# Kernel optimization log

Measured on AMD Instinct MI355X. Metric: run time of the kernel, lower is better.

The kernel has to match this reference:

```python
import jax, jax.numpy as jnp
import numpy as np

B, S, D = 32, 256, 768
H = 12
HD = D // H           # 64
MLP = 4 * D           # 3072
EPS = 1e-5


def layernorm(x, g, b):
    mu = jnp.mean(x, axis=-1, keepdims=True)
    var = jnp.mean((x - mu) ** 2, axis=-1, keepdims=True)
    return (x - mu) * jax.lax.rsqrt(var + EPS) * g + b


def setup_inputs() -> dict:
    key = jax.random.key(0)
    ks = jax.random.split(key, 16)
    s_head = 1.0 / np.sqrt(HD)
    s_d = 1.0 / np.sqrt(D)
    s_mlp = 1.0 / np.sqrt(MLP)
    return {
        "x": jax.random.normal(ks[0], (B, S, D), dtype=jnp.float32),
        "g1": jnp.ones((D,), jnp.float32),
        "beta1": jnp.zeros((D,), jnp.float32),
        # per-head linear weights, torch Linear layout [out, in] stacked over heads
        "Wq": jax.random.uniform(ks[1], (H, HD, HD), jnp.float32, -s_head, s_head),
        "bq": jax.random.uniform(ks[2], (H, HD), jnp.float32, -s_head, s_head),
        "Wk": jax.random.uniform(ks[3], (H, HD, HD), jnp.float32, -s_head, s_head),
        "bk": jax.random.uniform(ks[4], (H, HD), jnp.float32, -s_head, s_head),
        "Wv": jax.random.uniform(ks[5], (H, HD, HD), jnp.float32, -s_head, s_head),
        "bv": jax.random.uniform(ks[6], (H, HD), jnp.float32, -s_head, s_head),
        "g2": jnp.ones((D,), jnp.float32),
        "beta2": jnp.zeros((D,), jnp.float32),
        "W1": jax.random.uniform(ks[7], (MLP, D), jnp.float32, -s_d, s_d),
        "bm1": jax.random.uniform(ks[8], (MLP,), jnp.float32, -s_d, s_d),
        "W2": jax.random.uniform(ks[9], (D, MLP), jnp.float32, -s_mlp, s_mlp),
        "bm2": jax.random.uniform(ks[10], (D,), jnp.float32, -s_mlp, s_mlp),
    }


def reference(x, g1, beta1, Wq, bq, Wk, bk, Wv, bv, g2, beta2, W1, bm1, W2, bm2):
    # --- MHA on norm1(x), fused over batch and heads ---
    h = layernorm(x, g1, beta1)                      # [B,S,D]
    hh = h.reshape(B, S, H, HD)                      # head split matches slicing in Mymha
    # q_e = sum_d hh_d * W[e,d]  (torch Linear: y = x @ W.T + b)
    q = jnp.einsum('bshd,hed->bshe', hh, Wq) + bq
    k = jnp.einsum('bshd,hed->bshe', hh, Wk) + bk
    v = jnp.einsum('bshd,hed->bshe', hh, Wv) + bv
    scores = jnp.einsum('bshe,bthe->bhst', q, k) / np.sqrt(HD)
    attn = jax.nn.softmax(scores, axis=-1)           # [B,H,S,S]
    ctx = jnp.einsum('bhst,bthe->bshe', attn, v).reshape(B, S, D)
    out = ctx + x
    # --- MLP on norm2(out) ---
    h2 = layernorm(out, g2, beta2)
    m = jax.nn.gelu(h2 @ W1.T + bm1, approximate=False)  # torch nn.GELU is exact erf
    out = m @ W2.T + bm2 + out
    return out
```

## Files before the change

### kernel.cpp

```cpp
#include <hip/hip_runtime.h>
#include <hip/hip_bf16.h>
#include <math.h>


static constexpr int Bn = 32, Sn = 256, Dn = 768, Hn = 12, HDn = 64, MLPn = 3072;
static constexpr int NT = Bn * Sn;

typedef unsigned short ushort_t;
typedef unsigned int u32;
typedef __attribute__((ext_vector_type(8))) short short8;
typedef __attribute__((ext_vector_type(4))) float f32x4;

__device__ __forceinline__ float bf2f(ushort_t u) { return __uint_as_float(((u32)u) << 16); }
__device__ __forceinline__ ushort_t f2bf(float f) {
  u32 u = __float_as_uint(f);
  u += 0x7fffu + ((u >> 16) & 1u);
  return (ushort_t)(u >> 16);
}

__device__ __forceinline__ void async_cp16(const ushort_t* g, ushort_t* l) {
  __builtin_amdgcn_global_load_lds(
      (const __attribute__((address_space(1))) u32*)g,
      (__attribute__((address_space(3))) u32*)l, 16, 0, 0);
}

__global__ __launch_bounds__(256) void k_prep(
    const float* __restrict__ Wq, const float* __restrict__ Wk,
    const float* __restrict__ Wv, const float* __restrict__ bq,
    const float* __restrict__ bk, const float* __restrict__ bv,
    const float* __restrict__ W1, const float* __restrict__ W2,
    const float* __restrict__ x, const float* __restrict__ g1,
    const float* __restrict__ be1,
    ushort_t* __restrict__ Wc, float* __restrict__ bc,
    ushort_t* __restrict__ W1b, ushort_t* __restrict__ W2b,
    ushort_t* __restrict__ hb)
{
  __shared__ float red[8];
  const int bx = blockIdx.x;
  const int tid = threadIdx.x;
  if (bx < 576) {
    int i = bx * 256 + tid;
    int h = i / 12288, rem = i - h * 12288;
    int mat = rem / 4096, w = rem - mat * 4096;
    const float* src = (mat == 0) ? Wq : ((mat == 1) ? Wk : Wv);
    Wc[i] = f2bf(src[h * 4096 + w]);
    if (i < Hn * 192) {
      int h2 = i / 192, r2 = i - h2 * 192;
      int m2 = r2 / 64, e2 = r2 - m2 * 64;
      const float* bs = (m2 == 0) ? bq : ((m2 == 1) ? bk : bv);
      bc[i] = bs[h2 * 64 + e2];
    }
  } else if (bx < 5184) {
    int j = bx - 576;
    const float* src = (j < 2304) ? W1 : W2;
    ushort_t* dst = (j < 2304) ? W1b : W2b;
    int i = (j % 2304) * 256 + tid;
    float4 v = ((const float4*)src)[i];
    ushort4 o;
    o.x = f2bf(v.x); o.y = f2bf(v.y); o.z = f2bf(v.z); o.w = f2bf(v.w);
    ((ushort4*)dst)[i] = o;
  } else {
    const int t = bx - 5184;
    float xv[3];
#pragma unroll
    for (int i = 0; i < 3; i++) xv[i] = x[(size_t)t * Dn + tid + i * 256];
    float s = xv[0] + xv[1] + xv[2];
#pragma unroll
    for (int off = 32; off > 0; off >>= 1) s += __shfl_down(s, off, 64);
    if ((tid & 63) == 0) red[tid >> 6] = s;
    __syncthreads();
    float mean = (red[0] + red[1] + red[2] + red[3]) * (1.0f / 768.0f);
    float d0 = xv[0] - mean, d1 = xv[1] - mean, d2 = xv[2] - mean;
    float s2 = d0 * d0 + d1 * d1 + d2 * d2;
#pragma unroll
    for (int off = 32; off > 0; off >>= 1) s2 += __shfl_down(s2, off, 64);
    if ((tid & 63) == 0) red[4 + (tid >> 6)] = s2;
    __syncthreads();
    float rstd = rsqrtf((red[4] + red[5] + red[6] + red[7]) * (1.0f / 768.0f) + 1e-5f);
#pragma unroll
    for (int i = 0; i < 3; i++) {
      int d = tid + i * 256;
      hb[(size_t)t * Dn + d] = f2bf((xv[i] - mean) * rstd * g1[d] + be1[d]);
    }
  }
}

__global__ __launch_bounds__(256) void k_fused(
    const ushort_t* __restrict__ hb,
    const ushort_t* __restrict__ Wc,
    const float* __restrict__ bc,
    const float* __restrict__ x,
    float* __restrict__ out1)
{
  __shared__ __align__(16) ushort_t smem[77824];
  ushort_t* Qs  = smem;
  ushort_t* Ks  = smem + 16384;
  ushort_t* Vts = smem + 32768;
  ushort_t* As  = smem + 49152;
  ushort_t* Ws  = smem + 65536;
  ushort_t* Pw  = smem + 49152;

  const int bh = blockIdx.x;
  const int b_ = bh / Hn, h_ = bh - b_ * Hn;
  const int tid = threadIdx.x;
  const int wave = tid >> 6, lane = tid & 63;
  const int lrow = lane & 15, quad = lane >> 4;
  const int key = lrow & 7;
  const int t0 = b_ * Sn;

  {
    const ushort_t* ga = hb + (size_t)t0 * Dn + h_ * 64;
#pragma unroll
    for (int j = 0; j < 8; ++j) {
      int q = j * 256 + tid;
      int row = q >> 3;
      int sc = (q & 7) ^ (row & 7);
      async_cp16(ga + (size_t)row * Dn + sc * 8, As + q * 8);
    }
    const ushort_t* gw = Wc + h_ * 12288;
#pragma unroll
    for (int j = 0; j < 6; ++j) {
      int q = j * 256 + tid;
      int row = q >> 3;
      int sc = (q & 7) ^ (row & 7);
      async_cp16(gw + row * 64 + sc * 8, Ws + q * 8);
    }
  }
  asm volatile("s_waitcnt vmcnt(0)" ::: "memory");
  __syncthreads();

  const int wm = (wave >> 1) * 64, wn = (wave & 1) * 96;
  for (int half = 0; half < 2; ++half) {
    f32x4 acc[4][6];
#pragma unroll
    for (int mi = 0; mi < 4; mi++)
#pragma unroll
      for (int ni = 0; ni < 6; ni++) acc[mi][ni] = (f32x4){0.f, 0.f, 0.f, 0.f};

#pragma unroll
    for (int kk = 0; kk < 2; kk++) {
      short8 af[4], wf[6];
#pragma unroll
      for (int mi = 0; mi < 4; mi++)
        af[mi] = *(const short8*)(As + (half * 128 + wm + mi * 16 + lrow) * 64 + ((((kk << 2) + quad)) ^ key) * 8);
#pragma unroll
      for (int ni = 0; ni < 6; ni++)
        wf[ni] = *(const short8*)(Ws + (wn + ni * 16 + lrow) * 64 + ((((kk << 2) + quad)) ^ key) * 8);
#pragma unroll
      for (int mi = 0; mi < 4; mi++)
#pragma unroll
        for (int ni = 0; ni < 6; ni++)
          acc[mi][ni] = __builtin_amdgcn_mfma_f32_16x16x32_bf16(af[mi], wf[ni], acc[mi][ni], 0, 0, 0);
    }

#pragma unroll
    for (int ni = 0; ni < 6; ni++) {
      int c = wn + ni * 16 + lrow;
      int mat = c >> 6, e = c & 63;
      float bb = bc[h_ * 192 + c];
      if (mat < 2) {
        ushort_t* dst = (mat == 0) ? Qs : Ks;
#pragma unroll
        for (int mi = 0; mi < 4; mi++) {
#pragma unroll
          for (int r = 0; r < 4; r++) {
            int srow = half * 128 + wm + mi * 16 + quad * 4 + r;
            dst[srow * 64 + (((e >> 3) ^ (srow & 7)) << 3) + (e & 7)] = f2bf(acc[mi][ni][r] + bb);
          }
        }
      } else {
#pragma unroll
        for (int mi = 0; mi < 4; mi++) {
          int c4 = half * 128 + wm + mi * 16 + quad * 4;
          ushort4 pk;
          pk.x = f2bf(acc[mi][ni][0] + bb);
          pk.y = f2bf(acc[mi][ni][1] + bb);
          pk.z = f2bf(acc[mi][ni][2] + bb);
          pk.w = f2bf(acc[mi][ni][3] + bb);
          int cq = c4 >> 3;
          *(ushort4*)(Vts + e * 256 + ((cq ^ (e & 7)) << 3) + (c4 & 7)) = pk;
        }
      }
    }
  }
  __syncthreads();

  ushort_t* Pme = Pw + wave * 4224;
  for (int p = 0; p < 4; ++p) {
    const int s0 = wave * 64 + p * 16;
    short8 qf[2];
#pragma unroll
    for (int kk = 0; kk < 2; kk++)
      qf[kk] = *(const short8*)(Qs + (s0 + lrow) * 64 + ((((kk << 2) + quad)) ^ key) * 8);

    f32x4 sc[16];
#pragma unroll
    for (int ni = 0; ni < 16; ni++) sc[ni] = (f32x4){0.f, 0.f, 0.f, 0.f};
#pragma unroll
    for (int kk = 0; kk < 2; kk++) {
#pragma unroll
      for (int ni = 0; ni < 16; ni++) {
        short8 kf = *(const short8*)(Ks + (ni * 16 + lrow) * 64 + ((((kk << 2) + quad)) ^ key) * 8);
        sc[ni] = __builtin_amdgcn_mfma_f32_16x16x32_bf16(qf[kk], kf, sc[ni], 0, 0, 0);
      }
    }

    float inv[4];
#pragma unroll
    for (int r = 0; r < 4; r++) {
      float m_ = sc[0][r];
#pragma unroll
      for (int ni = 1; ni < 16; ni++) m_ = fmaxf(m_, sc[ni][r]);
#pragma unroll
      for (int msk = 8; msk >= 1; msk >>= 1) m_ = fmaxf(m_, __shfl_xor(m_, msk, 64));
      float s_ = 0.f;
#pragma unroll
      for (int ni = 0; ni < 16; ni++) {
        float pv = __expf((sc[ni][r] - m_) * 0.125f);
        s_ += pv;
        Pme[(quad * 4 + r) * 264 + ni * 16 + lrow] = f2bf(pv);
      }
#pragma unroll
      for (int msk = 8; msk >= 1; msk >>= 1) s_ += __shfl_xor(s_, msk, 64);
      inv[r] = 1.0f / s_;
    }
    asm volatile("s_waitcnt lgkmcnt(0)" ::: "memory");
    __builtin_amdgcn_sched_barrier(0);

    f32x4 of[4];
#pragma unroll
    for (int et = 0; et < 4; et++) of[et] = (f32x4){0.f, 0.f, 0.f, 0.f};
#pragma unroll
    for (int ks = 0; ks < 8; ks++) {
      short8 pf = *(const short8*)(Pme + lrow * 264 + ks * 32 + quad * 8);
#pragma unroll
      for (int et = 0; et < 4; et++) {
        short8 vf = *(const short8*)(Vts + (et * 16 + lrow) * 256 + ((((ks << 2) + quad)) ^ key) * 8);
        of[et] = __builtin_amdgcn_mfma_f32_16x16x32_bf16(pf, vf, of[et], 0, 0, 0);
      }
    }

    const size_t obase = ((size_t)t0 + s0) * Dn + h_ * 64;
#pragma unroll
    for (int r = 0; r < 4; r++) {
      float rl = inv[r];
      int row = quad * 4 + r;
#pragma unroll
      for (int et = 0; et < 4; et++) {
        size_t idx = obase + (size_t)row * Dn + et * 16 + lrow;
        out1[idx] = of[et][r] * rl + x[idx];
      }
    }
  }
}

__global__ __launch_bounds__(256) void k_ln2(
    const float* __restrict__ in, const float* __restrict__ g2,
    const float* __restrict__ be2, ushort_t* __restrict__ h2)
{
  const int t = blockIdx.x, tid = threadIdx.x;
  __shared__ float red[8];
  float xv[3];
#pragma unroll
  for (int i = 0; i < 3; i++) xv[i] = in[(size_t)t * Dn + tid + i * 256];
  float s = xv[0] + xv[1] + xv[2];
#pragma unroll
  for (int off = 32; off > 0; off >>= 1) s += __shfl_down(s, off, 64);
  if ((tid & 63) == 0) red[tid >> 6] = s;
  __syncthreads();
  float mean = (red[0] + red[1] + red[2] + red[3]) * (1.0f / 768.0f);
  float d0 = xv[0] - mean, d1 = xv[1] - mean, d2 = xv[2] - mean;
  float s2 = d0 * d0 + d1 * d1 + d2 * d2;
#pragma unroll
  for (int off = 32; off > 0; off >>= 1) s2 += __shfl_down(s2, off, 64);
  if ((tid & 63) == 0) red[4 + (tid >> 6)] = s2;
  __syncthreads();
  float rstd = rsqrtf((red[4] + red[5] + red[6] + red[7]) * (1.0f / 768.0f) + 1e-5f);
#pragma unroll
  for (int i = 0; i < 3; i++) {
    int d = tid + i * 256;
    h2[(size_t)t * Dn + d] = f2bf((xv[i] - mean) * rstd * g2[d] + be2[d]);
  }
}

__global__ __launch_bounds__(512, 2) void k_gemm1(
    const ushort_t* __restrict__ A,
    const ushort_t* __restrict__ Bw,
    const float* __restrict__ bias,
    ushort_t* __restrict__ CoutB)
{
  constexpr int KD = Dn;
  constexpr int NTILES = 12;
  constexpr int BUFU = 28672;
  __shared__ __align__(16) ushort_t smem[57344];
  const int b = blockIdx.x;
  const int xcd = b & 7, slot = b >> 3;
  const int cc = slot % 16, rloc = slot / 16;
  const int m0 = (xcd * 4 + rloc) * 256, n0 = cc * 192;
  const int tid = threadIdx.x;
  const int wave = tid >> 6, lane = tid & 63;
  const int wm2 = (wave >> 2) * 128, wn2 = (wave & 3) * 48;
  const int lrow = lane & 15, quad = lane >> 4;
  const int key = lrow & 7;

  f32x4 acc[8][3];
#pragma unroll
  for (int mi = 0; mi < 8; mi++)
#pragma unroll
    for (int ni = 0; ni < 3; ni++) acc[mi][ni] = (f32x4){0.f, 0.f, 0.f, 0.f};

  auto stageA = [&](int t, int half) {
    if (t >= NTILES) return;
    const int k0 = t * 64;
    ushort_t* tb = smem + (t & 1) * BUFU + half * 8192;
#pragma unroll
    for (int j = 0; j < 2; ++j) {
      int q = j * 512 + tid;
      int row = q >> 3;
      int sc = (q & 7) ^ (row & 7);
      async_cp16(A + (size_t)(m0 + half * 128 + row) * KD + k0 + sc * 8, tb + q * 8);
    }
  };
  auto stageB = [&](int t) {
    if (t >= NTILES) return;
    const int k0 = t * 64;
    ushort_t* tb = smem + (t & 1) * BUFU + 16384;
#pragma unroll
    for (int j = 0; j < 3; ++j) {
      int q = j * 512 + tid;
      int row = q >> 3;
      int sc = (q & 7) ^ (row & 7);
      async_cp16(Bw + (size_t)(n0 + row) * KD + k0 + sc * 8, tb + q * 8);
    }
  };

  stageA(0, 0); stageA(0, 1); stageB(0);
  asm volatile("s_waitcnt vmcnt(0)" ::: "memory");
  __builtin_amdgcn_s_barrier();
  __builtin_amdgcn_sched_barrier(0);

  short8 af[4][2], af2[4][2], bf0[3], bf1[3];
  for (int t = 0; t < NTILES; ++t) {
    const ushort_t* Ab = smem + (t & 1) * BUFU;
    const ushort_t* Bb = Ab + 16384;

#pragma unroll
    for (int mi = 0; mi < 4; ++mi)
#pragma unroll
      for (int kk = 0; kk < 2; ++kk)
        af[mi][kk] = *(const short8*)(Ab + (wm2 + mi * 16 + lrow) * 64 + (((kk << 2) + quad) ^ key) * 8);
#pragma unroll
    for (int ni = 0; ni < 3; ++ni)
      bf0[ni] = *(const short8*)(Bb + (wn2 + ni * 16 + lrow) * 64 + ((quad ^ key) * 8));
    stageA(t + 1, 0);
    __builtin_amdgcn_s_barrier();
    asm volatile("s_waitcnt lgkmcnt(0)" ::: "memory");
    __builtin_amdgcn_sched_barrier(0);
    __builtin_amdgcn_s_setprio(1);
#pragma unroll
    for (int mi = 0; mi < 4; ++mi)
#pragma unroll
      for (int ni = 0; ni < 3; ++ni)
        acc[mi][ni] = __builtin_amdgcn_mfma_f32_16x16x32_bf16(af[mi][0], bf0[ni], acc[mi][ni], 0, 0, 0);
    __builtin_amdgcn_s_setprio(0);
    __builtin_amdgcn_s_barrier();
    __builtin_amdgcn_sched_barrier(0);

#pragma unroll
    for (int ni = 0; ni < 3; ++ni)
      bf1[ni] = *(const short8*)(Bb + (wn2 + ni * 16 + lrow) * 64 + (((4 + quad) ^ key) * 8));
#pragma unroll
    for (int mi = 0; mi < 4; ++mi)
#pragma unroll
      for (int kk = 0; kk < 2; ++kk)
        af2[mi][kk] = *(const short8*)(Ab + (wm2 + 64 + mi * 16 + lrow) * 64 + (((kk << 2) + quad) ^ key) * 8);
    stageA(t + 1, 1);
    __builtin_amdgcn_s_barrier();
    asm volatile("s_waitcnt lgkmcnt(0)" ::: "memory");
    __builtin_amdgcn_sched_barrier(0);
    __builtin_amdgcn_s_setprio(1);
#pragma unroll
    for (int mi = 0; mi < 4; ++mi)
#pragma unroll
      for (int ni = 0; ni < 3; ++ni)
        acc[mi][ni] = __builtin_amdgcn_mfma_f32_16x16x32_bf16(af[mi][1], bf1[ni], acc[mi][ni], 0, 0, 0);
    __builtin_amdgcn_s_setprio(0);
    __builtin_amdgcn_s_barrier();
    __builtin_amdgcn_sched_barrier(0);

    stageB(t + 1);
    __builtin_amdgcn_s_barrier();
    __builtin_amdgcn_sched_barrier(0);
    __builtin_amdgcn_s_setprio(1);
#pragma unroll
    for (int mi = 0; mi < 4; ++mi)
#pragma unroll
      for (int ni = 0; ni < 3; ++ni)
        acc[4 + mi][ni] = __builtin_amdgcn_mfma_f32_16x16x32_bf16(af2[mi][0], bf0[ni], acc[4 + mi][ni], 0, 0, 0);
    __builtin_amdgcn_s_setprio(0);
    __builtin_amdgcn_s_barrier();
    __builtin_amdgcn_sched_barrier(0);

    __builtin_amdgcn_s_setprio(1);
#pragma unroll
    for (int mi = 0; mi < 4; ++mi)
#pragma unroll
      for (int ni = 0; ni < 3; ++ni)
        acc[4 + mi][ni] = __builtin_amdgcn_mfma_f32_16x16x32_bf16(af2[mi][1], bf1[ni], acc[4 + mi][ni], 0, 0, 0);
    __builtin_amdgcn_s_setprio(0);
    asm volatile("s_waitcnt vmcnt(0)" ::: "memory");
    __builtin_amdgcn_s_barrier();
    __builtin_amdgcn_sched_barrier(0);
  }

  float bwv[3];
#pragma unroll
  for (int ni = 0; ni < 3; ++ni) bwv[ni] = bias[n0 + wn2 + ni * 16 + lrow];
  __syncthreads();
#pragma unroll
  for (int mi = 0; mi < 8; ++mi) {
#pragma unroll
    for (int ni = 0; ni < 3; ++ni) {
      int col = wn2 + ni * 16 + lrow;
#pragma unroll
      for (int r = 0; r < 4; ++r) {
        int row = wm2 + mi * 16 + quad * 4 + r;
        float vv = acc[mi][ni][r] + bwv[ni];
        float u = vv * (0.7978845608f + 0.0356774081f * vv * vv);
        float o = vv / (1.0f + __expf(-2.0f * u));
        smem[row * 200 + col] = f2bf(o);
      }
    }
  }
  __syncthreads();
#pragma unroll
  for (int i = 0; i < 12; ++i) {
    int idx = i * 512 + tid;
    int rr = idx / 24, ck = idx - rr * 24;
    const uint4 v = *(const uint4*)(smem + rr * 200 + ck * 8);
    *(uint4*)(CoutB + (size_t)(m0 + rr) * MLPn + n0 + ck * 8) = v;
  }
}

__global__ __launch_bounds__(512, 2) void k_gemm2(
    const ushort_t* __restrict__ A,
    const ushort_t* __restrict__ Bw,
    const float* __restrict__ bias,
    const float* __restrict__ res,
    float* __restrict__ out)
{
  constexpr int KD = MLPn;
  constexpr int N = Dn;
  constexpr int NTILES = 48;
  constexpr int BUFU = 20480;
  __shared__ __align__(16) ushort_t smem[61440];
  const int b = blockIdx.x;
  const int xcd = b & 7, slot = b >> 3;
  const int cc = slot & 3, rloc = slot >> 2;
  const int m0 = (xcd * 8 + rloc) * 128, n0 = cc * 192;
  const int tid = threadIdx.x;
  const int wave = tid >> 6, lane = tid & 63;
  const int wm2 = (wave >> 2) * 64, wn2 = (wave & 3) * 48;
  const int lrow = lane & 15, quad = lane >> 4;
  const int key = lrow & 7;

  f32x4 acc[4][3];
#pragma unroll
  for (int mi = 0; mi < 4; mi++)
#pragma unroll
    for (int ni = 0; ni < 3; ni++) acc[mi][ni] = (f32x4){0.f, 0.f, 0.f, 0.f};

  auto stageT = [&](int t) {
    if (t >= NTILES) return;
    const int k0 = t * 64;
    ushort_t* bufA = smem + (t % 3) * BUFU;
    ushort_t* bufB = bufA + 8192;
#pragma unroll
    for (int j = 0; j < 2; ++j) {
      int q = j * 512 + tid;
      int row = q >> 3;
      int sc = (q & 7) ^ (row & 7);
      async_cp16(A + (size_t)(m0 + row) * KD + k0 + sc * 8, bufA + q * 8);
    }
#pragma unroll
    for (int j = 0; j < 3; ++j) {
      int q = j * 512 + tid;
      int row = q >> 3;
      int sc = (q & 7) ^ (row & 7);
      async_cp16(Bw + (size_t)(n0 + row) * KD + k0 + sc * 8, bufB + q * 8);
    }
  };

  stageT(0); stageT(1);
  asm volatile("s_waitcnt vmcnt(5)" ::: "memory");
  __builtin_amdgcn_s_barrier();
  __builtin_amdgcn_sched_barrier(0);

  short8 af[4], bf[3];
  for (int t = 0; t < NTILES; ++t) {
    const ushort_t* Ab = smem + (t % 3) * BUFU;
    const ushort_t* Bb = Ab + 8192;

#pragma unroll
    for (int mi = 0; mi < 4; ++mi)
      af[mi] = *(const short8*)(Ab + (wm2 + mi * 16 + lrow) * 64 + ((quad ^ key) * 8));
#pragma unroll
    for (int ni = 0; ni < 3; ++ni)
      bf[ni] = *(const short8*)(Bb + (wn2 + ni * 16 + lrow) * 64 + ((quad ^ key) * 8));
    stageT(t + 2);
    asm volatile("s_waitcnt lgkmcnt(0)" ::: "memory");
    __builtin_amdgcn_sched_barrier(0);
    __builtin_amdgcn_s_setprio(1);
#pragma unroll
    for (int mi = 0; mi < 4; ++mi)
#pragma unroll
      for (int ni = 0; ni < 3; ++ni)
        acc[mi][ni] = __builtin_amdgcn_mfma_f32_16x16x32_bf16(af[mi], bf[ni], acc[mi][ni], 0, 0, 0);
    __builtin_amdgcn_s_setprio(0);
#pragma unroll
    for (int mi = 0; mi < 4; ++mi)
      af[mi] = *(const short8*)(Ab + (wm2 + mi * 16 + lrow) * 64 + (((4 + quad) ^ key) * 8));
#pragma unroll
    for (int ni = 0; ni < 3; ++ni)
      bf[ni] = *(const short8*)(Bb + (wn2 + ni * 16 + lrow) * 64 + (((4 + quad) ^ key) * 8));
    asm volatile("s_waitcnt lgkmcnt(0)" ::: "memory");
    __builtin_amdgcn_sched_barrier(0);
    __builtin_amdgcn_s_setprio(1);
#pragma unroll
    for (int mi = 0; mi < 4; ++mi)
#pragma unroll
      for (int ni = 0; ni < 3; ++ni)
        acc[mi][ni] = __builtin_amdgcn_mfma_f32_16x16x32_bf16(af[mi], bf[ni], acc[mi][ni], 0, 0, 0);
    __builtin_amdgcn_s_setprio(0);
    if (t < NTILES - 2) {
      asm volatile("s_waitcnt vmcnt(5)" ::: "memory");
    } else {
      asm volatile("s_waitcnt vmcnt(0)" ::: "memory");
    }
    __builtin_amdgcn_s_barrier();
    __builtin_amdgcn_sched_barrier(0);
  }

#pragma unroll
  for (int ni = 0; ni < 3; ++ni) {
    int col = n0 + wn2 + ni * 16 + lrow;
    float bc = bias[col];
#pragma unroll
    for (int mi = 0; mi < 4; ++mi) {
#pragma unroll
      for (int r = 0; r < 4; ++r) {
        int row = m0 + wm2 + mi * 16 + quad * 4 + r;
        size_t idx = (size_t)row * N + col;
        out[idx] = acc[mi][ni][r] + bc + res[idx];
      }
    }
  }
}

extern "C" void kernel_launch(void* const* d_in, const int* in_sizes, int n_in,
                              void* d_out, int out_size, void* d_ws, size_t ws_size,
                              hipStream_t stream) {
  (void)in_sizes; (void)n_in; (void)out_size; (void)ws_size;
  const float* x   = (const float*)d_in[0];
  const float* g1  = (const float*)d_in[1];
  const float* be1 = (const float*)d_in[2];
  const float* Wq  = (const float*)d_in[3];
  const float* bq  = (const float*)d_in[4];
  const float* Wk  = (const float*)d_in[5];
  const float* bk  = (const float*)d_in[6];
  const float* Wv  = (const float*)d_in[7];
  const float* bv  = (const float*)d_in[8];
  const float* g2  = (const float*)d_in[9];
  const float* be2 = (const float*)d_in[10];
  const float* W1  = (const float*)d_in[11];
  const float* bm1 = (const float*)d_in[12];
  const float* W2  = (const float*)d_in[13];
  const float* bm2 = (const float*)d_in[14];
  float* outp = (float*)d_out;

  char* ws = (char*)d_ws;
  float*    out1 = (float*)ws;
  ushort_t* hb   = (ushort_t*)(ws + 25165824);
  ushort_t* h2   = (ushort_t*)(ws + 25165824);
  ushort_t* mb   = (ushort_t*)(ws + 37748736);
  ushort_t* Wc   = (ushort_t*)(ws + 88080384);
  ushort_t* W1b  = (ushort_t*)(ws + 88375296);
  ushort_t* W2b  = (ushort_t*)(ws + 93093888);
  float*    bcb  = (float*)(ws + 97812480);

  k_prep<<<dim3(5184 + NT), dim3(256), 0, stream>>>(Wq, Wk, Wv, bq, bk, bv, W1, W2,
                                                    x, g1, be1, Wc, bcb, W1b, W2b, hb);
  k_fused<<<dim3(Bn * Hn), dim3(256), 0, stream>>>(hb, Wc, bcb, x, out1);
  k_ln2<<<dim3(NT), dim3(256), 0, stream>>>(out1, g2, be2, h2);
  k_gemm1<<<dim3(512), dim3(512), 0, stream>>>(h2, W1b, bm1, mb);
  k_gemm2<<<dim3(256), dim3(512), 0, stream>>>(mb, W2b, bm2, out1, outp);
}
```

Baseline: 267.9 us.

## Halve GEMM1 row tile and switch to triple-buffered prefetch-two pipeline

The first MLP GEMM now uses a 128x192 output tile instead of 256x192, with twice as many blocks. Its K loop moves from a double-buffered schedule with split A/B staging and many barriers to a three-stage LDS ring. Loads for tile t+2 are issued while tile t is computed, with a partial vmcnt wait and one barrier per iteration. The aim is to hide global-load latency, cut synchronisation and improve load balance across CUs. The cost is lower data reuse per block, since each W1 tile is loaded by twice as many blocks, and a larger LDS footprint.

```diff
diff --git a/kernel.cpp b/kernel.cpp
--- a/kernel.cpp
+++ b/kernel.cpp
@@ -291,134 +291,100 @@
 {
   constexpr int KD = Dn;
   constexpr int NTILES = 12;
-  constexpr int BUFU = 28672;
-  __shared__ __align__(16) ushort_t smem[57344];
+  constexpr int BUFU = 20480;
+  __shared__ __align__(16) ushort_t smem[61440];
   const int b = blockIdx.x;
   const int xcd = b & 7, slot = b >> 3;
   const int cc = slot % 16, rloc = slot / 16;
-  const int m0 = (xcd * 4 + rloc) * 256, n0 = cc * 192;
+  const int m0 = (xcd * 8 + rloc) * 128, n0 = cc * 192;
   const int tid = threadIdx.x;
   const int wave = tid >> 6, lane = tid & 63;
-  const int wm2 = (wave >> 2) * 128, wn2 = (wave & 3) * 48;
+  const int wm2 = (wave >> 2) * 64, wn2 = (wave & 3) * 48;
   const int lrow = lane & 15, quad = lane >> 4;
   const int key = lrow & 7;
 
-  f32x4 acc[8][3];
-#pragma unroll
-  for (int mi = 0; mi < 8; mi++)
+  f32x4 acc[4][3];
+#pragma unroll
+  for (int mi = 0; mi < 4; mi++)
 #pragma unroll
     for (int ni = 0; ni < 3; ni++) acc[mi][ni] = (f32x4){0.f, 0.f, 0.f, 0.f};
 
-  auto stageA = [&](int t, int half) {
+  auto stageT = [&](int t) {
     if (t >= NTILES) return;
     const int k0 = t * 64;
-    ushort_t* tb = smem + (t & 1) * BUFU + half * 8192;
+    ushort_t* bufA = smem + (t % 3) * BUFU;
+    ushort_t* bufB = bufA + 8192;
 #pragma unroll
     for (int j = 0; j < 2; ++j) {
       int q = j * 512 + tid;
       int row = q >> 3;
       int sc = (q & 7) ^ (row & 7);
-      async_cp16(A + (size_t)(m0 + half * 128 + row) * KD + k0 + sc * 8, tb + q * 8);
-    }
-  };
-  auto stageB = [&](int t) {
-    if (t >= NTILES) return;
-    const int k0 = t * 64;
-    ushort_t* tb = smem + (t & 1) * BUFU + 16384;
+      async_cp16(A + (size_t)(m0 + row) * KD + k0 + sc * 8, bufA + q * 8);
+    }
 #pragma unroll
     for (int j = 0; j < 3; ++j) {
       int q = j * 512 + tid;
       int row = q >> 3;
       int sc = (q & 7) ^ (row & 7);
-      async_cp16(Bw + (size_t)(n0 + row) * KD + k0 + sc * 8, tb + q * 8);
+      async_cp16(Bw + (size_t)(n0 + row) * KD + k0 + sc * 8, bufB + q * 8);
     }
   };
 
-  stageA(0, 0); stageA(0, 1); stageB(0);
-  asm volatile("s_waitcnt vmcnt(0)" ::: "memory");
+  stageT(0); stageT(1);
+  asm volatile("s_waitcnt vmcnt(5)" ::: "memory");
   __builtin_amdgcn_s_barrier();
   __builtin_amdgcn_sched_barrier(0);
 
-  short8 af[4][2], af2[4][2], bf0[3], bf1[3];
+  short8 af[4], bf[3];
   for (int t = 0; t < NTILES; ++t) {
-    const ushort_t* Ab = smem + (t & 1) * BUFU;
-    const ushort_t* Bb = Ab + 16384;
-
-#pragma unroll
-    for (int mi = 0; mi < 4; ++mi)
-#pragma unroll
-      for (int kk = 0; kk < 2; ++kk)
-        af[mi][kk] = *(const short8*)(Ab + (wm2 + mi * 16 + lrow) * 64 + (((kk << 2) + quad) ^ key) * 8);
+    const ushort_t* Ab = smem + (t % 3) * BUFU;
+    const ushort_t* Bb = Ab + 8192;
+
+#pragma unroll
+    for (int mi = 0; mi < 4; ++mi)
+      af[mi] = *(const short8*)(Ab + (wm2 + mi * 16 + lrow) * 64 + ((quad ^ key) * 8));
 #pragma unroll
     for (int ni = 0; ni < 3; ++ni)
-      bf0[ni] = *(const short8*)(Bb + (wn2 + ni * 16 + lrow) * 64 + ((quad ^ key) * 8));
-    stageA(t + 1, 0);
+      bf[ni] = *(const short8*)(Bb + (wn2 + ni * 16 + lrow) * 64 + ((quad ^ key) * 8));
+    stageT(t + 2);
+    asm volatile("s_waitcnt lgkmcnt(0)" ::: "memory");
+    __builtin_amdgcn_sched_barrier(0);
+    __builtin_amdgcn_s_setprio(1);
+#pragma unroll
+    for (int mi = 0; mi < 4; ++mi)
+#pragma unroll
+      for (int ni = 0; ni < 3; ++ni)
+        acc[mi][ni] = __builtin_amdgcn_mfma_f32_16x16x32_bf16(af[mi], bf[ni], acc[mi][ni], 0, 0, 0);
+    __builtin_amdgcn_s_setprio(0);
+#pragma unroll
+    for (int mi = 0; mi < 4; ++mi)
+      af[mi] = *(const short8*)(Ab + (wm2 + mi * 16 + lrow) * 64 + (((4 + quad) ^ key) * 8));
+#pragma unroll
+    for (int ni = 0; ni < 3; ++ni)
+      bf[ni] = *(const short8*)(Bb + (wn2 + ni * 16 + lrow) * 64 + (((4 + quad) ^ key) * 8));
+    asm volatile("s_waitcnt lgkmcnt(0)" ::: "memory");
+    __builtin_amdgcn_sched_barrier(0);
+    __builtin_amdgcn_s_setprio(1);
+#pragma unroll
+    for (int mi = 0; mi < 4; ++mi)
+#pragma unroll
+      for (int ni = 0; ni < 3; ++ni)
+        acc[mi][ni] = __builtin_amdgcn_mfma_f32_16x16x32_bf16(af[mi], bf[ni], acc[mi][ni], 0, 0, 0);
+    __builtin_amdgcn_s_setprio(0);
+    if (t < NTILES - 2) {
+      asm volatile("s_waitcnt vmcnt(5)" ::: "memory");
+    } else {
+      asm volatile("s_waitcnt vmcnt(0)" ::: "memory");
+    }
     __builtin_amdgcn_s_barrier();
-    asm volatile("s_waitcnt lgkmcnt(0)" ::: "memory");
-    __builtin_amdgcn_sched_barrier(0);
-    __builtin_amdgcn_s_setprio(1);
-#pragma unroll
-    for (int mi = 0; mi < 4; ++mi)
-#pragma unroll
-      for (int ni = 0; ni < 3; ++ni)
-        acc[mi][ni] = __builtin_amdgcn_mfma_f32_16x16x32_bf16(af[mi][0], bf0[ni], acc[mi][ni], 0, 0, 0);
-    __builtin_amdgcn_s_setprio(0);
-    __builtin_amdgcn_s_barrier();
-    __builtin_amdgcn_sched_barrier(0);
-
-#pragma unroll
-    for (int ni = 0; ni < 3; ++ni)
-      bf1[ni] = *(const short8*)(Bb + (wn2 + ni * 16 + lrow) * 64 + (((4 + quad) ^ key) * 8));
-#pragma unroll
-    for (int mi = 0; mi < 4; ++mi)
-#pragma unroll
-      for (int kk = 0; kk < 2; ++kk)
-        af2[mi][kk] = *(const short8*)(Ab + (wm2 + 64 + mi * 16 + lrow) * 64 + (((kk << 2) + quad) ^ key) * 8);
-    stageA(t + 1, 1);
-    __builtin_amdgcn_s_barrier();
-    asm volatile("s_waitcnt lgkmcnt(0)" ::: "memory");
-    __builtin_amdgcn_sched_barrier(0);
-    __builtin_amdgcn_s_setprio(1);
-#pragma unroll
-    for (int mi = 0; mi < 4; ++mi)
-#pragma unroll
-      for (int ni = 0; ni < 3; ++ni)
-        acc[mi][ni] = __builtin_amdgcn_mfma_f32_16x16x32_bf16(af[mi][1], bf1[ni], acc[mi][ni], 0, 0, 0);
-    __builtin_amdgcn_s_setprio(0);
-    __builtin_amdgcn_s_barrier();
-    __builtin_amdgcn_sched_barrier(0);
-
-    stageB(t + 1);
-    __builtin_amdgcn_s_barrier();
-    __builtin_amdgcn_sched_barrier(0);
-    __builtin_amdgcn_s_setprio(1);
-#pragma unroll
-    for (int mi = 0; mi < 4; ++mi)
-#pragma unroll
-      for (int ni = 0; ni < 3; ++ni)
-        acc[4 + mi][ni] = __builtin_amdgcn_mfma_f32_16x16x32_bf16(af2[mi][0], bf0[ni], acc[4 + mi][ni], 0, 0, 0);
-    __builtin_amdgcn_s_setprio(0);
-    __builtin_amdgcn_s_barrier();
-    __builtin_amdgcn_sched_barrier(0);
-
-    __builtin_amdgcn_s_setprio(1);
-#pragma unroll
-    for (int mi = 0; mi < 4; ++mi)
-#pragma unroll
-      for (int ni = 0; ni < 3; ++ni)
-        acc[4 + mi][ni] = __builtin_amdgcn_mfma_f32_16x16x32_bf16(af2[mi][1], bf1[ni], acc[4 + mi][ni], 0, 0, 0);
-    __builtin_amdgcn_s_setprio(0);
-    asm volatile("s_waitcnt vmcnt(0)" ::: "memory");
-    __builtin_amdgcn_s_barrier();
     __builtin_amdgcn_sched_barrier(0);
   }
 
   float bwv[3];
 #pragma unroll
   for (int ni = 0; ni < 3; ++ni) bwv[ni] = bias[n0 + wn2 + ni * 16 + lrow];
-  __syncthreads();
-#pragma unroll
-  for (int mi = 0; mi < 8; ++mi) {
+#pragma unroll
+  for (int mi = 0; mi < 4; ++mi) {
 #pragma unroll
     for (int ni = 0; ni < 3; ++ni) {
       int col = wn2 + ni * 16 + lrow;
@@ -434,7 +400,7 @@
   }
   __syncthreads();
 #pragma unroll
-  for (int i = 0; i < 12; ++i) {
+  for (int i = 0; i < 6; ++i) {
     int idx = i * 512 + tid;
     int rr = idx / 24, ck = idx - rr * 24;
     const uint4 v = *(const uint4*)(smem + rr * 200 + ck * 8);
@@ -592,6 +558,6 @@
                                                     x, g1, be1, Wc, bcb, W1b, W2b, hb);
   k_fused<<<dim3(Bn * Hn), dim3(256), 0, stream>>>(hb, Wc, bcb, x, out1);
   k_ln2<<<dim3(NT), dim3(256), 0, stream>>>(out1, g2, be2, h2);
-  k_gemm1<<<dim3(512), dim3(512), 0, stream>>>(h2, W1b, bm1, mb);
+  k_gemm1<<<dim3(1024), dim3(512), 0, stream>>>(h2, W1b, bm1, mb);
   k_gemm2<<<dim3(256), dim3(512), 0, stream>>>(mb, W2b, bm2, out1, outp);
 }
```

Measured after the change: 272.4 us. About the same (+1.7%).
